# Kernel optimization log

Hardware: AMD Instinct MI355X
Metric: run time of the kernel (lower is better)

Reference implementation:

```python
import jax, jax.numpy as jnp
import numpy as np

N_NODES = 1_000_000
N_EDGES = 16_000_000


def setup_inputs() -> dict:
    key = jax.random.key(0)
    ks = jax.random.split(key, 12)
    x = jax.random.normal(ks[0], (N_NODES, 3), dtype=jnp.float32)
    edge_index = jax.random.randint(ks[1], (2, N_EDGES), 0, N_NODES, dtype=jnp.int64)
    # GCNConv uses Linear(in, out, bias=False) + separate post-aggregation bias
    def lin(k, fi, fo):
        return jax.random.normal(k, (fi, fo), dtype=jnp.float32) / np.sqrt(fi)
    W1 = lin(ks[2], 3, 4); b1 = jnp.zeros((4,), jnp.float32)
    W2 = lin(ks[3], 4, 4); b2 = jnp.zeros((4,), jnp.float32)
    W3 = lin(ks[4], 4, 3); b3 = jnp.zeros((3,), jnp.float32)
    Wc = lin(ks[5], 3, 5)
    bc = jax.random.normal(ks[6], (5,), dtype=jnp.float32) * 0.01
    return {"x": x, "edge_index": edge_index, "W1": W1, "b1": b1,
            "W2": W2, "b2": b2, "W3": W3, "b3": b3, "Wc": Wc, "bc": bc}


def reference(x, edge_index, W1, b1, W2, b2, W3, b3, Wc, bc):
    N = x.shape[0]
    loop = jnp.arange(N, dtype=edge_index.dtype)
    row = jnp.concatenate([edge_index[0], loop])  # source (with self-loops)
    col = jnp.concatenate([edge_index[1], loop])  # target (with self-loops)
    # symmetric GCN normalization: deg over targets incl. self-loops
    deg = jax.ops.segment_sum(jnp.ones_like(row, dtype=x.dtype), col, num_segments=N)
    dinv = jnp.where(deg > 0, jax.lax.rsqrt(deg), 0.0)
    norm = dinv[row] * dinv[col]  # [E+N]

    def gcn_conv(h, W, b):
        h = h @ W                              # [N, F_out]
        msg = norm[:, None] * h[row]           # gather + scale, [E+N, F_out]
        agg = jax.ops.segment_sum(msg, col, num_segments=N)
        return agg + b

    h = jnp.tanh(gcn_conv(x, W1, b1))
    h = jnp.tanh(gcn_conv(h, W2, b2))
    h = jnp.tanh(gcn_conv(h, W3, b3))
    out = h @ Wc + bc
    return (out, h)
```

## Files before the change

kernel.cpp:

```cpp
#include <hip/hip_runtime.h>


#define BKT_BITS 10
#define BKT_SZ   1024
#define MAXK     2048
#define TILE     8192
#define HTILE    4096
#define CHUNK    32768
#define TPC      4
#define SEGC     32
#define MAXSEG   32
#define ATHR     1024
#define RECSENT  0xFFFFFFFFu

typedef int v4i __attribute__((ext_vector_type(4)));

constexpr float XD_SCALE = 4096.0f;
constexpr float HD_SCALE = 16384.0f;
constexpr int   QBIAS    = 1 << 17;

__device__ __forceinline__ short q16(float v, float s) {
    int t = __float2int_rn(v * s);
    t = max(-32767, min(32767, t));
    return (short)t;
}

__device__ __forceinline__ void ld_tile(const int* __restrict__ p, long t0, long t1,
                                        int tid, int4* dst, int sentinel) {
#pragma unroll
    for (int v = 0; v < 2; ++v) {
        long e = t0 + (long)v * HTILE + (long)tid * 4;
        if (e + 3 < t1) {
            dst[v] = *(const int4*)(p + e);
        } else {
            int* d = (int*)&dst[v];
#pragma unroll
            for (int j = 0; j < 4; ++j) d[j] = (e + j < t1) ? p[e + j] : sentinel;
        }
    }
}

__global__ __launch_bounds__(ATHR) void k_hist(const int* __restrict__ row,
                                               const int* __restrict__ col, int E,
                                               unsigned short* __restrict__ cnt16,
                                               unsigned half, int NB) {
    __shared__ unsigned lh[MAXK];
    lh[threadIdx.x] = 0u; lh[threadIdx.x + 1024] = 0u;
    __syncthreads();
    long e0 = (long)blockIdx.x * TILE;
    long e1 = e0 + TILE; if (e1 > E) e1 = E;
    int4 c4[2], r4[2];
    ld_tile(col, e0, e1, threadIdx.x, c4, -1);
    ld_tile(row, e0, e1, threadIdx.x, r4, 0);
#pragma unroll
    for (int v = 0; v < 2; ++v) {
        const int* cc = (const int*)&c4[v];
        const int* rr = (const int*)&r4[v];
#pragma unroll
        for (int j = 0; j < 4; ++j) {
            unsigned b = ((unsigned)cc[j]) >> BKT_BITS;
            if (b < (unsigned)NB) {
                unsigned key = (b << 1) | (((unsigned)rr[j] >= half) ? 1u : 0u);
                atomicAdd(&lh[key], 1u);
            }
        }
    }
    __syncthreads();
    cnt16[(size_t)blockIdx.x * MAXK + threadIdx.x] = (unsigned short)lh[threadIdx.x];
    cnt16[(size_t)blockIdx.x * MAXK + threadIdx.x + 1024] =
        (unsigned short)lh[threadIdx.x + 1024];
}

__global__ __launch_bounds__(256) void k_offA(const unsigned short* __restrict__ cnt16,
                                              int ntile, unsigned* __restrict__ psum) {
    int seg = blockIdx.x >> 3;
    int k = ((blockIdx.x & 7) << 8) + threadIdx.x;
    int tlo = seg * SEGC * TPC;
    int thi = (seg + 1) * SEGC * TPC; if (thi > ntile) thi = ntile;
    unsigned s = 0;
    for (int t = tlo; t < thi; ++t) s += cnt16[(size_t)t * MAXK + k];
    psum[(size_t)seg * MAXK + k] = s;
}

__global__ __launch_bounds__(256) void k_totB(const unsigned* __restrict__ psum, int nseg,
                                              unsigned* __restrict__ kcnt) {
    int k = blockIdx.x * blockDim.x + threadIdx.x;
    unsigned s = 0;
    for (int g = 0; g < nseg; ++g) s += psum[(size_t)g * MAXK + k];
    kcnt[k] = s;
}

__global__ __launch_bounds__(1024) void k_scan2(const unsigned* __restrict__ kcnt,
                                                unsigned* __restrict__ kpfx) {
    __shared__ unsigned tot[MAXK], pfx[MAXK];
    int t = threadIdx.x;
    tot[t] = kcnt[t]; tot[t + 1024] = kcnt[t + 1024];
    __syncthreads();
    if (t == 0) {
        unsigned run = 0;
        for (int i = 0; i < MAXK; ++i) { pfx[i] = run; run += tot[i]; }
    }
    __syncthreads();
    kpfx[t] = pfx[t]; kpfx[t + 1024] = pfx[t + 1024];
}

__global__ __launch_bounds__(1024) void k_offB(unsigned* __restrict__ psum, int nseg,
                                               const unsigned* __restrict__ kpfx) {
    for (int k = threadIdx.x; k < MAXK; k += 1024) {
        unsigned run = kpfx[k];
        for (int g = 0; g < nseg; ++g) {
            unsigned t = psum[(size_t)g * MAXK + k];
            psum[(size_t)g * MAXK + k] = run;
            run += t;
        }
    }
}

__global__ __launch_bounds__(256) void k_offC(const unsigned short* __restrict__ cnt16,
                                              int ntile,
                                              const unsigned* __restrict__ psum,
                                              unsigned* __restrict__ offs, int nblk) {
    int seg = blockIdx.x >> 3;
    int k = ((blockIdx.x & 7) << 8) + threadIdx.x;
    int clo = seg * SEGC;
    int chi = clo + SEGC; if (chi > nblk) chi = nblk;
    unsigned run = psum[(size_t)seg * MAXK + k];
    for (int c = clo; c < chi; ++c) {
        offs[(size_t)c * MAXK + k] = run;
        int tlo = c * TPC, thi = tlo + TPC; if (thi > ntile) thi = ntile;
        for (int t = tlo; t < thi; ++t) run += cnt16[(size_t)t * MAXK + k];
    }
}

__global__ __launch_bounds__(ATHR, 8) void k_place(const int* __restrict__ row,
                                                   const int* __restrict__ col, int E,
                                                   const unsigned* __restrict__ offs,
                                                   const unsigned short* __restrict__ cnt16,
                                                   unsigned* __restrict__ recbuf,
                                                   unsigned half, int NB) {
    __shared__ unsigned lo[MAXK], cnt[MAXK], sc[MAXK], pc[MAXK];
    __shared__ unsigned rec[TILE];
    __shared__ unsigned short bkt[TILE];
    int tid = threadIdx.x, lane = tid & 63, wid = tid >> 6;
    lo[tid]        = offs[(size_t)blockIdx.x * MAXK + tid];
    lo[tid + 1024] = offs[(size_t)blockIdx.x * MAXK + tid + 1024];
    long base = (long)blockIdx.x * CHUNK;
    long bend = base + CHUNK; if (bend > E) bend = E;
    int ntl = (int)((bend - base + TILE - 1) / TILE);
    int4 fc[2], fr[2];
    {
        long t1 = min(base + TILE, bend);
        ld_tile(col, base, t1, tid, fc, -1);
        ld_tile(row, base, t1, tid, fr, 0);
    }
    for (int ti = 0; ti < ntl; ++ti) {
        unsigned c0 = (unsigned)cnt16[(size_t)(blockIdx.x * TPC + ti) * MAXK + tid * 2];
        unsigned c1 = (unsigned)cnt16[(size_t)(blockIdx.x * TPC + ti) * MAXK + tid * 2 + 1];
        unsigned s = c0 + c1;
        unsigned v = s;
#pragma unroll
        for (int d = 1; d < 64; d <<= 1) {
            unsigned t = __shfl_up(v, d);
            if (lane >= d) v += t;
        }
        if (lane == 63) pc[wid] = v;
        __syncthreads();
        if (tid < 16) {
            unsigned w = pc[tid];
            unsigned iw = w;
#pragma unroll
            for (int d = 1; d < 16; d <<= 1) {
                unsigned t = __shfl_up(iw, d, 16);
                if (tid >= d) iw += t;
            }
            pc[tid] = iw - w;
        }
        __syncthreads();
        unsigned tbase = pc[wid] + (v - s);
        sc[tid * 2]     = tbase;
        sc[tid * 2 + 1] = tbase + c0;
        cnt[tid * 2]     = c0;
        cnt[tid * 2 + 1] = c1;
        __syncthreads();
        pc[tid] = 0u; pc[tid + 1024] = 0u;
        __syncthreads();
        int4 cc4[2] = {fc[0], fc[1]};
        int4 cr4[2] = {fr[0], fr[1]};
#pragma unroll
        for (int vv = 0; vv < 2; ++vv) {
            const int* cc = (const int*)&cc4[vv];
            const int* rr = (const int*)&cr4[vv];
#pragma unroll
            for (int j = 0; j < 4; ++j) {
                unsigned c = (unsigned)cc[j];
                unsigned b = c >> BKT_BITS;
                if (b >= (unsigned)NB) continue;
                unsigned r = (unsigned)rr[j];
                unsigned key = (b << 1) | ((r >= half) ? 1u : 0u);
                unsigned pos = sc[key] + atomicAdd(&pc[key], 1u);
                rec[pos] = (r << BKT_BITS) | (c & (BKT_SZ - 1));
                bkt[pos] = (unsigned short)key;
            }
        }
        __syncthreads();
        unsigned total = sc[MAXK - 1] + cnt[MAXK - 1];
        if (ti + 1 < ntl) {
            long n0 = base + (long)(ti + 1) * TILE;
            long n1 = min(n0 + TILE, bend);
            ld_tile(col, n0, n1, tid, fc, -1);
            ld_tile(row, n0, n1, tid, fr, 0);
        }
        for (unsigned t = tid; t < total; t += ATHR) {
            unsigned k = bkt[t];
            recbuf[(size_t)lo[k] + (t - sc[k])] = rec[t];
        }
        __syncthreads();
        lo[tid] += cnt[tid];
        lo[tid + 1024] += cnt[tid + 1024];
        __syncthreads();
    }
}

__global__ __launch_bounds__(ATHR) void k_bcount(const unsigned* __restrict__ recbuf,
                                                 const unsigned* __restrict__ kpfx,
                                                 const unsigned* __restrict__ kcnt,
                                                 const float* __restrict__ x,
                                                 unsigned short* __restrict__ deg,
                                                 short4* __restrict__ bufA, int N) {
    __shared__ unsigned cnt[BKT_SZ];
    int b = blockIdx.x;
    cnt[threadIdx.x] = 0u;
    __syncthreads();
#pragma unroll
    for (int h = 0; h < 2; ++h) {
        unsigned seg = ((unsigned)b << 1) | (unsigned)h;
        unsigned st = kpfx[seg], n = kcnt[seg];
        for (unsigned j = threadIdx.x; j < n; j += blockDim.x)
            atomicAdd(&cnt[recbuf[(size_t)st + j] & (BKT_SZ - 1)], 1u);
    }
    __syncthreads();
    int node = (b << BKT_BITS) + threadIdx.x;
    if (node < N) {
        unsigned short d16 = (unsigned short)cnt[threadIdx.x];
        deg[node] = d16;
        float dv = rsqrtf((float)d16 + 1.0f);
        short4 o;
        o.x = q16(dv * x[(long)node*3 + 0], XD_SCALE);
        o.y = q16(dv * x[(long)node*3 + 1], XD_SCALE);
        o.z = q16(dv * x[(long)node*3 + 2], XD_SCALE);
        o.w = 0;
        bufA[node] = o;
    }
}

template <int FIN, int FOUT, bool OUT_DINV, int PHASE>
__global__ __launch_bounds__(ATHR) void k_bpass(const unsigned* __restrict__ recbuf,
                                                const unsigned* __restrict__ kpfx,
                                                const unsigned* __restrict__ kcnt,
                                                const short4* __restrict__ bufIn,
                                                float inv_s,
                                                const unsigned short* __restrict__ deg,
                                                const float* __restrict__ W,
                                                const float* __restrict__ bias,
                                                short4* __restrict__ bufOut,
                                                unsigned long long* __restrict__ accg,
                                                int N) {
    __shared__ unsigned long long acc[BKT_SZ][2];
    int b = blockIdx.x;
    int nodeT = (b << BKT_BITS) + threadIdx.x;
    if (PHASE == 2) {
        acc[threadIdx.x][0] = accg[(size_t)nodeT * 2 + 0];
        acc[threadIdx.x][1] = accg[(size_t)nodeT * 2 + 1];
    } else {
        acc[threadIdx.x][0] = 0ull; acc[threadIdx.x][1] = 0ull;
    }
    __syncthreads();
    unsigned seg = ((unsigned)b << 1) | (unsigned)(PHASE - 1);
    unsigned start = kpfx[seg], n = kcnt[seg];
    unsigned lim = start + n;
    unsigned abase = start & ~3u;
    unsigned tot4 = lim - abase;
    for (unsigned j = (unsigned)threadIdx.x * 4u; j < tot4; j += ATHR * 4u) {
        unsigned idx = abase + j;
        unsigned r0, r1, r2, r3;
        if (idx >= start && idx + 4u <= lim) {
            v4i r = __builtin_nontemporal_load((const v4i*)(recbuf + idx));
            r0 = (unsigned)r.x; r1 = (unsigned)r.y;
            r2 = (unsigned)r.z; r3 = (unsigned)r.w;
        } else {
            unsigned rr[4];
#pragma unroll
            for (int k = 0; k < 4; ++k) {
                unsigned ii = idx + (unsigned)k;
                rr[k] = (ii >= start && ii < lim) ? recbuf[ii] : RECSENT;
            }
            r0 = rr[0]; r1 = rr[1]; r2 = rr[2]; r3 = rr[3];
        }
        short4 q0, q1, q2, q3;
        if (r0 != RECSENT) q0 = bufIn[r0 >> BKT_BITS];
        if (r1 != RECSENT) q1 = bufIn[r1 >> BKT_BITS];
        if (r2 != RECSENT) q2 = bufIn[r2 >> BKT_BITS];
        if (r3 != RECSENT) q3 = bufIn[r3 >> BKT_BITS];
#define BP_ACC(rv, qv)                                                          \
        if (rv != RECSENT) {                                                    \
            unsigned nl = rv & (BKT_SZ - 1);                                    \
            unsigned long long v0 =                                             \
                ((unsigned long long)(unsigned)(qv.y + QBIAS) << 32)            \
              |  (unsigned long long)(unsigned)(qv.x + QBIAS);                  \
            atomicAdd(&acc[nl][0], v0);                                         \
            if (FIN > 2) {                                                      \
                unsigned long long v1 =                                         \
                    ((unsigned long long)(unsigned)(qv.w + QBIAS) << 32)        \
                  |  (unsigned long long)(unsigned)(qv.z + QBIAS);              \
                atomicAdd(&acc[nl][1], v1);                                     \
            }                                                                   \
        }
        BP_ACC(r0, q0) BP_ACC(r1, q1) BP_ACC(r2, q2) BP_ACC(r3, q3)
#undef BP_ACC
    }
    __syncthreads();
    if (PHASE == 1) {
        accg[(size_t)nodeT * 2 + 0] = acc[threadIdx.x][0];
        accg[(size_t)nodeT * 2 + 1] = acc[threadIdx.x][1];
        return;
    }
    int node = nodeT;
    if (node >= N) return;
    int dgi = (int)deg[node];
    long long db = (long long)dgi * QBIAS;
    float dv = rsqrtf((float)dgi + 1.0f);
    short4 qs = bufIn[node];
    unsigned long long a0_ = acc[threadIdx.x][0];
    unsigned long long a1_ = acc[threadIdx.x][1];
    float s[4] = {0.f, 0.f, 0.f, 0.f};
    s[0] = (float)((long long)(unsigned)(a0_)        - db + qs.x) * inv_s;
    s[1] = (float)((long long)(unsigned)(a0_ >> 32)  - db + qs.y) * inv_s;
    if (FIN > 2) {
        s[2] = (float)((long long)(unsigned)(a1_)       - db + qs.z) * inv_s;
        s[3] = (float)((long long)(unsigned)(a1_ >> 32) - db + qs.w) * inv_s;
    }
    float o[4] = {0.f, 0.f, 0.f, 0.f};
#pragma unroll
    for (int fo = 0; fo < FOUT; ++fo) {
        float t = 0.f;
#pragma unroll
        for (int fi = 0; fi < FIN; ++fi) t += s[fi] * W[fi * FOUT + fo];
        o[fo] = tanhf(dv * t + bias[fo]);
    }
    float m = OUT_DINV ? dv : 1.0f;
    short4 outv;
    outv.x = q16(o[0] * m, HD_SCALE);
    outv.y = q16(o[1] * m, HD_SCALE);
    outv.z = (FOUT > 2) ? q16(o[2] * m, HD_SCALE) : (short)0;
    outv.w = (FOUT > 3) ? q16(o[3] * m, HD_SCALE) : (short)0;
    bufOut[node] = outv;
}

__global__ __launch_bounds__(256) void k_final(const short4* __restrict__ h3q,
                                               const float* __restrict__ Wc,
                                               const float* __restrict__ bc,
                                               float* __restrict__ out,
                                               float* __restrict__ hout, int n) {
    int i = blockIdx.x * blockDim.x + threadIdx.x;
    if (i >= n) return;
    short4 q = h3q[i];
    float h0 = (float)q.x * (1.0f / HD_SCALE);
    float h1 = (float)q.y * (1.0f / HD_SCALE);
    float h2 = (float)q.z * (1.0f / HD_SCALE);
    hout[(long)i*3 + 0] = h0;
    hout[(long)i*3 + 1] = h1;
    hout[(long)i*3 + 2] = h2;
#pragma unroll
    for (int k = 0; k < 5; ++k)
        out[(long)i*5 + k] = h0 * Wc[k] + h1 * Wc[5 + k] + h2 * Wc[10 + k] + bc[k];
}

extern "C" void kernel_launch(void* const* d_in, const int* in_sizes, int n_in,
                              void* d_out, int out_size, void* d_ws, size_t ws_size,
                              hipStream_t stream) {
    const float* x   = (const float*)d_in[0];
    const int*   ei  = (const int*)d_in[1];
    const float* W1  = (const float*)d_in[2];
    const float* b1  = (const float*)d_in[3];
    const float* W2  = (const float*)d_in[4];
    const float* b2  = (const float*)d_in[5];
    const float* W3  = (const float*)d_in[6];
    const float* b3  = (const float*)d_in[7];
    const float* Wc  = (const float*)d_in[8];
    const float* bc  = (const float*)d_in[9];

    const int N = in_sizes[0] / 3;
    const int E = in_sizes[1] / 2;
    if (N > (1 << 20)) return;
    const int* row = ei;
    const int* col = ei + E;
    const int NB = (N + BKT_SZ - 1) >> BKT_BITS;
    const int ntile = (E + TILE - 1) / TILE;
    const int nblk  = (E + CHUNK - 1) / CHUNK;
    const int nseg  = (nblk + SEGC - 1) / SEGC;
    if (nseg > MAXSEG) return;
    const unsigned half = (unsigned)(N / 2);

    float* out  = (float*)d_out;
    float* hout = (float*)d_out + (long)N * 5;

    char* w0 = (char*)d_ws;
    char* w = w0;
    short4* bufA = (short4*)w;                      w += (size_t)N * 8;
    short4* bufB = (short4*)w;                      w += (size_t)N * 8;
    unsigned short* deg = (unsigned short*)w;       w += (size_t)N * 2;
    unsigned short* cnt16 = (unsigned short*)w;     w += (size_t)ntile * MAXK * 2;
    unsigned* offs  = (unsigned*)w;                 w += (size_t)nblk * MAXK * 4;
    unsigned* psum  = (unsigned*)w;                 w += (size_t)MAXSEG * MAXK * 4;
    unsigned* kpfx  = (unsigned*)w;                 w += (size_t)MAXK * 4;
    unsigned* kcnt  = (unsigned*)w;                 w += (size_t)MAXK * 4;
    unsigned long long* accg = (unsigned long long*)w;
    w += (size_t)NB * BKT_SZ * 16;
    unsigned* recbuf = (unsigned*)w;                w += (size_t)E * 4;
    if ((size_t)(w - w0) + 4096 > ws_size) return;

    const int BT = 256;
    const int gN = (N + BT - 1) / BT;

    k_hist<<<ntile, ATHR, 0, stream>>>(row, col, E, cnt16, half, NB);
    k_offA<<<nseg * 8, 256, 0, stream>>>(cnt16, ntile, psum);
    k_totB<<<8, 256, 0, stream>>>(psum, nseg, kcnt);
    k_scan2<<<1, 1024, 0, stream>>>(kcnt, kpfx);
    k_offB<<<1, 1024, 0, stream>>>(psum, nseg, kpfx);
    k_offC<<<nseg * 8, 256, 0, stream>>>(cnt16, ntile, psum, offs, nblk);
    k_place<<<nblk, ATHR, 0, stream>>>(row, col, E, offs, cnt16, recbuf, half, NB);
    k_bcount<<<NB, ATHR, 0, stream>>>(recbuf, kpfx, kcnt, x, deg, bufA, N);

#define RUN_BPASS(FIN, FOUT, ODV, BIN, ISC, WW, BB, BOUT)                          \
    k_bpass<FIN, FOUT, ODV, 1><<<NB, ATHR, 0, stream>>>(recbuf, kpfx, kcnt,        \
        BIN, ISC, deg, WW, BB, BOUT, accg, N);                                     \
    k_bpass<FIN, FOUT, ODV, 2><<<NB, ATHR, 0, stream>>>(recbuf, kpfx, kcnt,        \
        BIN, ISC, deg, WW, BB, BOUT, accg, N);

    RUN_BPASS(3, 4, true, bufA, 1.0f / XD_SCALE, W1, b1, bufB)
    RUN_BPASS(4, 4, true, bufB, 1.0f / HD_SCALE, W2, b2, bufA)
    RUN_BPASS(4, 3, false, bufA, 1.0f / HD_SCALE, W3, b3, bufB)
#undef RUN_BPASS

    k_final<<<gN, BT, 0, stream>>>(bufB, Wc, bc, out, hout, N);
}
```

Baseline: 494.9 us.

## Fuse final projection into last GCN pass, vectorize bcount and widen bpass loads

Removes the separate k_final kernel: the last aggregation pass now writes h and the classifier output directly from the float tanh results instead of round-tripping through a quantized buffer. k_bcount reads recbuf as 128-bit nontemporal vectors instead of scalar loads. k_bpass processes 8 records per thread per iteration instead of 4, giving more gathers in flight before the shared-memory atomics. The fused path also skips the final int16 quantization, slightly changing numerics, and the wider unroll raises register pressure.

Measured after the change: 497.6 us. No clear change (+0.6%).

```diff
diff --git a/kernel.cpp b/kernel.cpp
--- a/kernel.cpp
+++ b/kernel.cpp
@@ -235,8 +235,25 @@
     for (int h = 0; h < 2; ++h) {
         unsigned seg = ((unsigned)b << 1) | (unsigned)h;
         unsigned st = kpfx[seg], n = kcnt[seg];
-        for (unsigned j = threadIdx.x; j < n; j += blockDim.x)
-            atomicAdd(&cnt[recbuf[(size_t)st + j] & (BKT_SZ - 1)], 1u);
+        unsigned lim = st + n;
+        unsigned ab = st & ~3u;
+        for (unsigned j = (unsigned)threadIdx.x * 4u; j < lim - ab; j += ATHR * 4u) {
+            unsigned idx = ab + j;
+            if (idx >= st && idx + 4u <= lim) {
+                v4i r = __builtin_nontemporal_load((const v4i*)(recbuf + idx));
+                atomicAdd(&cnt[(unsigned)r.x & (BKT_SZ - 1)], 1u);
+                atomicAdd(&cnt[(unsigned)r.y & (BKT_SZ - 1)], 1u);
+                atomicAdd(&cnt[(unsigned)r.z & (BKT_SZ - 1)], 1u);
+                atomicAdd(&cnt[(unsigned)r.w & (BKT_SZ - 1)], 1u);
+            } else {
+#pragma unroll
+                for (int k = 0; k < 4; ++k) {
+                    unsigned ii = idx + (unsigned)k;
+                    if (ii >= st && ii < lim)
+                        atomicAdd(&cnt[recbuf[ii] & (BKT_SZ - 1)], 1u);
+                }
+            }
+        }
     }
     __syncthreads();
     int node = (b << BKT_BITS) + threadIdx.x;
@@ -253,7 +270,7 @@
     }
 }
 
-template <int FIN, int FOUT, bool OUT_DINV, int PHASE>
+template <int FIN, int FOUT, bool OUT_DINV, int PHASE, bool FINAL>
 __global__ __launch_bounds__(ATHR) void k_bpass(const unsigned* __restrict__ recbuf,
                                                 const unsigned* __restrict__ kpfx,
                                                 const unsigned* __restrict__ kcnt,
@@ -264,6 +281,10 @@
                                                 const float* __restrict__ bias,
                                                 short4* __restrict__ bufOut,
                                                 unsigned long long* __restrict__ accg,
+                                                const float* __restrict__ Wc,
+                                                const float* __restrict__ bc,
+                                                float* __restrict__ out,
+                                                float* __restrict__ hout,
                                                 int N) {
     __shared__ unsigned long long acc[BKT_SZ][2];
     int b = blockIdx.x;
@@ -279,44 +300,43 @@
     unsigned start = kpfx[seg], n = kcnt[seg];
     unsigned lim = start + n;
     unsigned abase = start & ~3u;
-    unsigned tot4 = lim - abase;
-    for (unsigned j = (unsigned)threadIdx.x * 4u; j < tot4; j += ATHR * 4u) {
+    unsigned tot = lim - abase;
+    for (unsigned j = (unsigned)threadIdx.x * 8u; j < tot; j += ATHR * 8u) {
         unsigned idx = abase + j;
-        unsigned r0, r1, r2, r3;
-        if (idx >= start && idx + 4u <= lim) {
-            v4i r = __builtin_nontemporal_load((const v4i*)(recbuf + idx));
-            r0 = (unsigned)r.x; r1 = (unsigned)r.y;
-            r2 = (unsigned)r.z; r3 = (unsigned)r.w;
+        unsigned r[8];
+        if (idx >= start && idx + 8u <= lim) {
+            v4i ra = __builtin_nontemporal_load((const v4i*)(recbuf + idx));
+            v4i rb = __builtin_nontemporal_load((const v4i*)(recbuf + idx + 4));
+            r[0] = (unsigned)ra.x; r[1] = (unsigned)ra.y;
+            r[2] = (unsigned)ra.z; r[3] = (unsigned)ra.w;
+            r[4] = (unsigned)rb.x; r[5] = (unsigned)rb.y;
+            r[6] = (unsigned)rb.z; r[7] = (unsigned)rb.w;
         } else {
-            unsigned rr[4];
-#pragma unroll
-            for (int k = 0; k < 4; ++k) {
+#pragma unroll
+            for (int k = 0; k < 8; ++k) {
                 unsigned ii = idx + (unsigned)k;
-                rr[k] = (ii >= start && ii < lim) ? recbuf[ii] : RECSENT;
-            }
-            r0 = rr[0]; r1 = rr[1]; r2 = rr[2]; r3 = rr[3];
-        }
-        short4 q0, q1, q2, q3;
-        if (r0 != RECSENT) q0 = bufIn[r0 >> BKT_BITS];
-        if (r1 != RECSENT) q1 = bufIn[r1 >> BKT_BITS];
-        if (r2 != RECSENT) q2 = bufIn[r2 >> BKT_BITS];
-        if (r3 != RECSENT) q3 = bufIn[r3 >> BKT_BITS];
-#define BP_ACC(rv, qv)                                                          \
-        if (rv != RECSENT) {                                                    \
-            unsigned nl = rv & (BKT_SZ - 1);                                    \
-            unsigned long long v0 =                                             \
-                ((unsigned long long)(unsigned)(qv.y + QBIAS) << 32)            \
-              |  (unsigned long long)(unsigned)(qv.x + QBIAS);                  \
-            atomicAdd(&acc[nl][0], v0);                                         \
-            if (FIN > 2) {                                                      \
-                unsigned long long v1 =                                         \
-                    ((unsigned long long)(unsigned)(qv.w + QBIAS) << 32)        \
-                  |  (unsigned long long)(unsigned)(qv.z + QBIAS);              \
-                atomicAdd(&acc[nl][1], v1);                                     \
-            }                                                                   \
-        }
-        BP_ACC(r0, q0) BP_ACC(r1, q1) BP_ACC(r2, q2) BP_ACC(r3, q3)
-#undef BP_ACC
+                r[k] = (ii >= start && ii < lim) ? recbuf[ii] : RECSENT;
+            }
+        }
+        short4 q[8];
+#pragma unroll
+        for (int k = 0; k < 8; ++k)
+            if (r[k] != RECSENT) q[k] = bufIn[r[k] >> BKT_BITS];
+#pragma unroll
+        for (int k = 0; k < 8; ++k) {
+            if (r[k] == RECSENT) continue;
+            unsigned nl = r[k] & (BKT_SZ - 1);
+            unsigned long long v0 =
+                ((unsigned long long)(unsigned)(q[k].y + QBIAS) << 32)
+              |  (unsigned long long)(unsigned)(q[k].x + QBIAS);
+            atomicAdd(&acc[nl][0], v0);
+            if (FIN > 2) {
+                unsigned long long v1 =
+                    ((unsigned long long)(unsigned)(q[k].w + QBIAS) << 32)
+                  |  (unsigned long long)(unsigned)(q[k].z + QBIAS);
+                atomicAdd(&acc[nl][1], v1);
+            }
+        }
     }
     __syncthreads();
     if (PHASE == 1) {
@@ -347,6 +367,15 @@
         for (int fi = 0; fi < FIN; ++fi) t += s[fi] * W[fi * FOUT + fo];
         o[fo] = tanhf(dv * t + bias[fo]);
     }
+    if (FINAL) {
+        hout[(long)node*3 + 0] = o[0];
+        hout[(long)node*3 + 1] = o[1];
+        hout[(long)node*3 + 2] = o[2];
+#pragma unroll
+        for (int k = 0; k < 5; ++k)
+            out[(long)node*5 + k] = o[0]*Wc[k] + o[1]*Wc[5+k] + o[2]*Wc[10+k] + bc[k];
+        return;
+    }
     float m = OUT_DINV ? dv : 1.0f;
     short4 outv;
     outv.x = q16(o[0] * m, HD_SCALE);
@@ -354,25 +383,6 @@
     outv.z = (FOUT > 2) ? q16(o[2] * m, HD_SCALE) : (short)0;
     outv.w = (FOUT > 3) ? q16(o[3] * m, HD_SCALE) : (short)0;
     bufOut[node] = outv;
-}
-
-__global__ __launch_bounds__(256) void k_final(const short4* __restrict__ h3q,
-                                               const float* __restrict__ Wc,
-                                               const float* __restrict__ bc,
-                                               float* __restrict__ out,
-                                               float* __restrict__ hout, int n) {
-    int i = blockIdx.x * blockDim.x + threadIdx.x;
-    if (i >= n) return;
-    short4 q = h3q[i];
-    float h0 = (float)q.x * (1.0f / HD_SCALE);
-    float h1 = (float)q.y * (1.0f / HD_SCALE);
-    float h2 = (float)q.z * (1.0f / HD_SCALE);
-    hout[(long)i*3 + 0] = h0;
-    hout[(long)i*3 + 1] = h1;
-    hout[(long)i*3 + 2] = h2;
-#pragma unroll
-    for (int k = 0; k < 5; ++k)
-        out[(long)i*5 + k] = h0 * Wc[k] + h1 * Wc[5 + k] + h2 * Wc[10 + k] + bc[k];
 }
 
 extern "C" void kernel_launch(void* const* d_in, const int* in_sizes, int n_in,
@@ -419,9 +429,6 @@
     unsigned* recbuf = (unsigned*)w;                w += (size_t)E * 4;
     if ((size_t)(w - w0) + 4096 > ws_size) return;
 
-    const int BT = 256;
-    const int gN = (N + BT - 1) / BT;
-
     k_hist<<<ntile, ATHR, 0, stream>>>(row, col, E, cnt16, half, NB);
     k_offA<<<nseg * 8, 256, 0, stream>>>(cnt16, ntile, psum);
     k_totB<<<8, 256, 0, stream>>>(psum, nseg, kcnt);
@@ -431,16 +438,14 @@
     k_place<<<nblk, ATHR, 0, stream>>>(row, col, E, offs, cnt16, recbuf, half, NB);
     k_bcount<<<NB, ATHR, 0, stream>>>(recbuf, kpfx, kcnt, x, deg, bufA, N);
 
-#define RUN_BPASS(FIN, FOUT, ODV, BIN, ISC, WW, BB, BOUT)                          \
-    k_bpass<FIN, FOUT, ODV, 1><<<NB, ATHR, 0, stream>>>(recbuf, kpfx, kcnt,        \
-        BIN, ISC, deg, WW, BB, BOUT, accg, N);                                     \
-    k_bpass<FIN, FOUT, ODV, 2><<<NB, ATHR, 0, stream>>>(recbuf, kpfx, kcnt,        \
-        BIN, ISC, deg, WW, BB, BOUT, accg, N);
-
-    RUN_BPASS(3, 4, true, bufA, 1.0f / XD_SCALE, W1, b1, bufB)
-    RUN_BPASS(4, 4, true, bufB, 1.0f / HD_SCALE, W2, b2, bufA)
-    RUN_BPASS(4, 3, false, bufA, 1.0f / HD_SCALE, W3, b3, bufB)
+#define RUN_BPASS(FIN, FOUT, ODV, FNL, BIN, ISC, WW, BB, BOUT)                     \
+    k_bpass<FIN, FOUT, ODV, 1, false><<<NB, ATHR, 0, stream>>>(recbuf, kpfx, kcnt, \
+        BIN, ISC, deg, WW, BB, BOUT, accg, Wc, bc, out, hout, N);                  \
+    k_bpass<FIN, FOUT, ODV, 2, FNL><<<NB, ATHR, 0, stream>>>(recbuf, kpfx, kcnt,   \
+        BIN, ISC, deg, WW, BB, BOUT, accg, Wc, bc, out, hout, N);
+
+    RUN_BPASS(3, 4, true, false, bufA, 1.0f / XD_SCALE, W1, b1, bufB)
+    RUN_BPASS(4, 4, true, false, bufB, 1.0f / HD_SCALE, W2, b2, bufA)
+    RUN_BPASS(4, 3, false, true, bufA, 1.0f / HD_SCALE, W3, b3, bufB)
 #undef RUN_BPASS
-
-    k_final<<<gN, BT, 0, stream>>>(bufB, Wc, bc, out, hout, N);
-}
+}
```
